# Kernel optimization log

Measured on AMD Instinct MI355X. Metric: run time of the kernel, lower is better.

Reference implementation:

```python
import jax, jax.numpy as jnp
import numpy as np

B, N, SIG_DIM, K = 128, 200000, 192, 32


def _l2norm(x):
    return x / jnp.linalg.norm(x, axis=-1, keepdims=True)


def setup_inputs() -> dict:
    key = jax.random.key(0)
    kq, kg, km = jax.random.split(key, 3)
    # queries and gallery signatures are L2-normalised per the docstring
    query_signature = _l2norm(jax.random.normal(kq, (B, SIG_DIM), dtype=jnp.float32))
    gallery_sigs = _l2norm(jax.random.normal(kg, (N, SIG_DIM), dtype=jnp.float32))
    exclude_mask = jax.random.bernoulli(km, p=0.01, shape=(B, N))
    return {
        "query_signature": query_signature,
        "gallery_sigs": gallery_sigs,
        "exclude_mask": exclude_mask,
        "k": K,
    }


def reference(query_signature, gallery_sigs, exclude_mask, k):
    # Equivalent to the chunked running top-k merge in Gallery.retrieve:
    # cosine-sim scores (inputs pre-normalised), masked fill -inf, global top-k.
    scores = query_signature @ gallery_sigs.T              # [B, N]
    scores = jnp.where(exclude_mask, -jnp.inf, scores)
    top_scores, top_idx = jax.lax.top_k(scores, k)          # [B, k] each
    return top_idx.astype(jnp.int64), top_scores
```

## Files before the change

kernel.cpp:

```cpp
#include <hip/hip_runtime.h>
#include <hip/hip_bf16.h>
#include <cstdint>
#include <cstddef>

#define BQ 128
#define DK 192
#define KTOP 32
#define CHI 32
#define QCAP 512
#define CAP 8192
#define OCAP 65536
#define MARGIN 0.02f
#define SCN 768
#define THRV 3200

#define NEG_INF (-__builtin_huge_valf())

typedef short short8v __attribute__((ext_vector_type(8)));
typedef float f32x16  __attribute__((ext_vector_type(16)));

__device__ __forceinline__ unsigned fkey(float s) {
    unsigned u = __float_as_uint(s);
    return (u & 0x80000000u) ? ~u : (u | 0x80000000u);
}
__device__ __forceinline__ bool pri_gt(float s1, int i1, float s2, int i2) {
    return (s1 > s2) || (s1 == s2 && i1 < i2);
}
__device__ __forceinline__ unsigned pk_trunc(float a, float b) {
    return __builtin_amdgcn_perm(__float_as_uint(b), __float_as_uint(a),
                                 0x07060302u);
}
__device__ __forceinline__ unsigned f2bf_rne(float x) {
    unsigned u = __float_as_uint(x);
    unsigned r = u + 0x7FFFu + ((u >> 16) & 1u);
    return r >> 16;
}
__device__ __forceinline__ float dot192(const float* __restrict__ a,
                                        const float* __restrict__ b) {
    float s = 0.f;
    #pragma unroll 8
    for (int k = 0; k < DK; ++k) s = fmaf(a[k], b[k], s);
    return s;
}
__device__ __forceinline__ void gload_lds16(const void* g, void* l) {
    __builtin_amdgcn_global_load_lds(
        (const __attribute__((address_space(1))) unsigned int*)g,
        (__attribute__((address_space(3))) unsigned int*)l,
        16, 0, 0);
}

__global__ __launch_bounds__(256) void qprep(
    const float* __restrict__ Qf, unsigned short* __restrict__ Qb)
{
    const int i = blockIdx.x * 256 + threadIdx.x;
    if (i < BQ * DK) Qb[i] = (unsigned short)f2bf_rne(Qf[i]);
}

template<int MODE>
__global__ __launch_bounds__(256, 2) void score_pass(
    const float* __restrict__ Qf, const unsigned short* __restrict__ Qb,
    const float* __restrict__ G,
    const int* __restrict__ mask, const float* __restrict__ thrm,
    float* __restrict__ gmax,
    int* __restrict__ gcnt, float* __restrict__ cs, int* __restrict__ ci,
    int* __restrict__ ocnt, int* __restrict__ oq, int* __restrict__ og,
    float* __restrict__ osv,
    int Ntot, int NCH, int SC)
{
    __shared__ float    Gf[CHI * DK];
    __shared__ float    thrmS[BQ];
    __shared__ unsigned queue[QCAP];
    __shared__ int      qn;

    const int t = threadIdx.x;
    const int w = t >> 6, lane = t & 63;
    const int lo5 = lane & 31, hi = lane >> 5;
    const int qbW = w * 32;

    const int chunk = (MODE == 0)
        ? (int)(((long long)blockIdx.x * NCH) / SC)
        : (int)blockIdx.x;
    const int cb = chunk * CHI;

    #pragma unroll
    for (int i = 0; i < 6; ++i) {
        const int slot = t + (i << 8);
        const int r = slot / 48, c = slot - r * 48;
        size_t grow = (size_t)cb + r;
        if (grow >= (size_t)Ntot) grow = (size_t)Ntot - 1;
        const char* gp = (const char*)G + grow * (DK * 4) + ((c ^ (r & 7)) << 4);
        char* lp = (char*)Gf + ((i << 2) + w) * 1024;
        gload_lds16(gp, lp);
    }

    uint4 aF[12];
    {
        const unsigned short* qp = Qb + (size_t)(qbW + lo5) * DK + hi * 8;
        #pragma unroll
        for (int s = 0; s < 12; ++s)
            aF[s] = *reinterpret_cast<const uint4*>(qp + s * 16);
    }

    if (t < BQ) thrmS[t] = (MODE == 1) ? thrm[t] : 0.f;
    if (t == 0) qn = 0;
    __syncthreads();

    const unsigned xsh = (unsigned)((lo5 & 7) << 4);
    const char* rowp = (const char*)Gf + lo5 * (DK * 4);

    f32x16 acc = {0,0,0,0,0,0,0,0,0,0,0,0,0,0,0,0};
    #pragma unroll
    for (int s = 0; s < 12; ++s) {
        const unsigned b0 = ((unsigned)((s * 4 + hi * 2) << 4)) ^ xsh;
        const unsigned b1 = ((unsigned)((s * 4 + hi * 2 + 1) << 4)) ^ xsh;
        float4 f0 = *reinterpret_cast<const float4*>(rowp + b0);
        float4 f1 = *reinterpret_cast<const float4*>(rowp + b1);
        union { unsigned u[4]; short8v v; } bu;
        bu.u[0] = pk_trunc(f0.x, f0.y); bu.u[1] = pk_trunc(f0.z, f0.w);
        bu.u[2] = pk_trunc(f1.x, f1.y); bu.u[3] = pk_trunc(f1.z, f1.w);
        union { uint4 u; short8v v; } au; au.u = aF[s];
        acc = __builtin_amdgcn_mfma_f32_32x32x16_bf16(au.v, bu.v, acc, 0, 0, 0);
    }

    const int g = cb + lo5;
    if (MODE == 0) {
        #pragma unroll
        for (int j = 0; j < 16; ++j) {
            const int row = (j & 3) + 8 * (j >> 2) + 4 * hi;
            const int q = qbW + row;
            float m = NEG_INF;
            if (g < Ntot && !mask[(size_t)q * (size_t)Ntot + g])
                m = acc[j];
            #pragma unroll
            for (int off = 1; off < 32; off <<= 1)
                m = fmaxf(m, __shfl_xor(m, off));
            if (lo5 == 0) gmax[(size_t)blockIdx.x * BQ + q] = m;
        }
    } else {
        #pragma unroll
        for (int j = 0; j < 16; ++j) {
            const int row = (j & 3) + 8 * (j >> 2) + 4 * hi;
            const int q = qbW + row;
            const float th = thrmS[q];
            const float s = acc[j];
            if (g < Ntot && s >= th) {
                if (!mask[(size_t)q * (size_t)Ntot + g]) {
                    const int p = atomicAdd(&qn, 1);
                    if (p < QCAP) {
                        queue[p] = ((unsigned)q << 24) | (unsigned)g;
                    } else {
                        float sx = dot192(Qf + q * DK, G + (size_t)g * DK);
                        const int op = atomicAdd(ocnt, 1);
                        if (op < OCAP) { oq[op] = q; og[op] = g; osv[op] = sx; }
                    }
                }
            }
        }
        __syncthreads();
        const int nq = qn < QCAP ? qn : QCAP;
        for (int cc = w; cc < nq; cc += 4) {
            const unsigned pk = queue[cc];
            const int q = pk >> 24, gg = pk & 0xFFFFFF;
            const float* qr = Qf + q * DK;
            const float* gr = G + (size_t)gg * DK;
            const int k0 = lane * 3;
            float part = qr[k0] * gr[k0];
            part = fmaf(qr[k0 + 1], gr[k0 + 1], part);
            part = fmaf(qr[k0 + 2], gr[k0 + 2], part);
            #pragma unroll
            for (int off = 32; off > 0; off >>= 1)
                part += __shfl_xor(part, off);
            if (lane == 0) {
                const int pos = atomicAdd(&gcnt[q * 16], 1);
                if (pos < CAP) {
                    cs[(size_t)q * CAP + pos] = part;
                    ci[(size_t)q * CAP + pos] = gg;
                } else {
                    const int op = atomicAdd(ocnt, 1);
                    if (op < OCAP) { oq[op] = q; og[op] = gg; osv[op] = part; }
                }
            }
        }
    }
}

__global__ __launch_bounds__(256) void thr32(
    const float* __restrict__ gmax, float* __restrict__ thrm, int SC)
{
    __shared__ float vals[THRV];
    __shared__ int hist[256];
    __shared__ int hscan[256];
    __shared__ int bS, gtS;

    const int q = blockIdx.x;
    const int t = threadIdx.x;
    const int M = SC < THRV ? SC : THRV;

    for (int i = t; i < M; i += 256) {
        float m = gmax[(size_t)i * BQ + q];
        for (int j = i + THRV; j < SC; j += THRV)
            m = fmaxf(m, gmax[(size_t)j * BQ + q]);
        vals[i] = m;
    }
    __syncthreads();

    unsigned prefix = 0, pmask = 0;
    int kneed = KTOP;
    for (int pass = 0; pass < 4; ++pass) {
        const int shift = 24 - pass * 8;
        hist[t] = 0;
        __syncthreads();
        for (int i = t; i < M; i += 256) {
            unsigned k = fkey(vals[i]);
            if ((k & pmask) == prefix) atomicAdd(&hist[(k >> shift) & 255], 1);
        }
        __syncthreads();
        int* src = hist; int* dst = hscan;
        for (int off = 1; off < 256; off <<= 1) {
            int v = src[t] + ((t + off) < 256 ? src[t + off] : 0);
            __syncthreads();
            dst[t] = v;
            __syncthreads();
            int* tmp = src; src = dst; dst = tmp;
        }
        if (src[t] >= kneed && (t == 255 || src[t + 1] < kneed)) {
            bS = t; gtS = (t == 255) ? 0 : src[t + 1];
        }
        __syncthreads();
        kneed -= gtS;
        prefix |= ((unsigned)bS) << shift;
        pmask  |= 0xFFu << shift;
        __syncthreads();
    }
    if (t == 0) {
        unsigned u = (prefix & 0x80000000u) ? (prefix & 0x7FFFFFFFu) : ~prefix;
        thrm[q] = __uint_as_float(u) - MARGIN;
    }
}

__global__ __launch_bounds__(256) void select_topk(
    const float* __restrict__ cs, const int* __restrict__ ci,
    const int* __restrict__ gcnt,
    const int* __restrict__ ocnt, const int* __restrict__ oq,
    const int* __restrict__ og, const float* __restrict__ osv,
    float* __restrict__ out)
{
    __shared__ int   hist[256];
    __shared__ int   hscan[256];
    __shared__ float Ls[256];
    __shared__ int   Li[256];
    __shared__ int   lcnt, nTotS, bS, gtS;
    __shared__ float wrs[4]; __shared__ int wri[4], wrslot[4];

    const int q = blockIdx.x;
    const int t = threadIdx.x;
    const int n0 = gcnt[q * 16];
    const int n = n0 < CAP ? n0 : CAP;
    const size_t base = (size_t)q * CAP;
    const int novf0 = *ocnt;
    const int novf = novf0 < OCAP ? novf0 : OCAP;

    if (t == 0) nTotS = 0;
    __syncthreads();
    {
        int part = (t == 0) ? n : 0;
        for (int i = t; i < novf; i += 256)
            if (oq[i] == q) part++;
        atomicAdd(&nTotS, part);
    }
    __syncthreads();
    const int nTot = nTotS;

    unsigned prefix = 0, pmask = 0;
    int kneed = KTOP;

    if (nTot > KTOP) {
        for (int pass = 0; pass < 4; ++pass) {
            const int shift = 24 - pass * 8;
            hist[t] = 0;
            __syncthreads();
            for (int i = t; i < n; i += 256) {
                unsigned k = fkey(cs[base + i]);
                if ((k & pmask) == prefix)
                    atomicAdd(&hist[(k >> shift) & 255], 1);
            }
            for (int i = t; i < novf; i += 256) {
                if (oq[i] == q) {
                    unsigned k = fkey(osv[i]);
                    if ((k & pmask) == prefix)
                        atomicAdd(&hist[(k >> shift) & 255], 1);
                }
            }
            __syncthreads();
            int* src = hist; int* dst = hscan;
            for (int off = 1; off < 256; off <<= 1) {
                int v = src[t] + ((t + off) < 256 ? src[t + off] : 0);
                __syncthreads();
                dst[t] = v;
                __syncthreads();
                int* tmp = src; src = dst; dst = tmp;
            }
            if (src[t] >= kneed && (t == 255 || src[t + 1] < kneed)) {
                bS = t;
                gtS = (t == 255) ? 0 : src[t + 1];
            }
            __syncthreads();
            const int b = bS;
            kneed -= gtS;
            prefix |= ((unsigned)b) << shift;
            pmask  |= 0xFFu << shift;
            __syncthreads();
        }
    }

    if (t == 0) lcnt = 0;
    __syncthreads();
    const unsigned T = (nTot > KTOP) ? prefix : 0u;
    for (int i = t; i < n; i += 256) {
        float s = cs[base + i];
        if (fkey(s) >= T) {
            int p = atomicAdd(&lcnt, 1);
            if (p < 256) { Ls[p] = s; Li[p] = ci[base + i]; }
        }
    }
    for (int i = t; i < novf; i += 256) {
        if (oq[i] == q) {
            float s = osv[i];
            if (fkey(s) >= T) {
                int p = atomicAdd(&lcnt, 1);
                if (p < 256) { Ls[p] = s; Li[p] = og[i]; }
            }
        }
    }
    __syncthreads();
    const int M = lcnt < 256 ? lcnt : 256;

    const int w = t >> 6, lane = t & 63;
    for (int r = 0; r < KTOP; ++r) {
        float bv = (t < M) ? Ls[t] : NEG_INF;
        int   bi = (t < M) ? Li[t] : 0x7fffffff;
        int   bslot = t;
        #pragma unroll
        for (int off = 32; off > 0; off >>= 1) {
            float ov = __shfl_xor(bv, off);
            int   oi = __shfl_xor(bi, off);
            int   osl = __shfl_xor(bslot, off);
            if (pri_gt(ov, oi, bv, bi)) { bv = ov; bi = oi; bslot = osl; }
        }
        if (lane == 0) { wrs[w] = bv; wri[w] = bi; wrslot[w] = bslot; }
        __syncthreads();
        if (t == 0) {
            float fv = wrs[0]; int fi = wri[0]; int fs = wrslot[0];
            #pragma unroll
            for (int ww = 1; ww < 4; ++ww)
                if (pri_gt(wrs[ww], wri[ww], fv, fi)) {
                    fv = wrs[ww]; fi = wri[ww]; fs = wrslot[ww];
                }
            out[q * KTOP + r]                     = (float)fi;
            out[(size_t)BQ * KTOP + q * KTOP + r] = fv;
            Ls[fs] = NEG_INF; Li[fs] = 0x7fffffff;
        }
        __syncthreads();
    }
}

extern "C" void kernel_launch(void* const* d_in, const int* in_sizes, int n_in,
                              void* d_out, int out_size, void* d_ws, size_t ws_size,
                              hipStream_t stream)
{
    const float* Qf   = (const float*)d_in[0];
    const float* G    = (const float*)d_in[1];
    const int*   mask = (const int*)d_in[2];
    const int Ntot = in_sizes[1] / DK;

    const int NCH = (Ntot + CHI - 1) / CHI;
    int SC = SCN;
    if (SC > NCH) SC = NCH;

    char* w = (char*)d_ws;
    int*   ocnt = (int*)(w + 0);
    int*   gcnt = (int*)(w + 1024);
    float* thrm = (float*)(w + 10240);
    unsigned short* Qb = (unsigned short*)(w + 16384);
    size_t off = 16384 + (size_t)BQ * DK * 2;
    off = (off + 255) & ~(size_t)255;
    float* gmax = (float*)(w + off);
    off += (size_t)SC * BQ * 4; off = (off + 255) & ~(size_t)255;
    float* cs   = (float*)(w + off);
    off += (size_t)BQ * CAP * 4;
    int*   ci   = (int*)(w + off);
    off += (size_t)BQ * CAP * 4;
    int*   oqv  = (int*)(w + off);   off += (size_t)OCAP * 4;
    int*   ogv  = (int*)(w + off);   off += (size_t)OCAP * 4;
    float* osv  = (float*)(w + off);

    (void)hipMemsetAsync(w, 0, 16384, stream);
    qprep<<<dim3((BQ * DK + 255) / 256), dim3(256), 0, stream>>>(Qf, Qb);
    score_pass<0><<<dim3(SC), dim3(256), 0, stream>>>(
        Qf, Qb, G, mask, thrm, gmax, gcnt, cs, ci, ocnt, oqv, ogv, osv,
        Ntot, NCH, SC);
    thr32<<<dim3(BQ), dim3(256), 0, stream>>>(gmax, thrm, SC);
    score_pass<1><<<dim3(NCH), dim3(256), 0, stream>>>(
        Qf, Qb, G, mask, thrm, gmax, gcnt, cs, ci, ocnt, oqv, ogv, osv,
        Ntot, NCH, SC);
    select_topk<<<dim3(BQ), dim3(256), 0, stream>>>(
        cs, ci, gcnt, ocnt, oqv, ogv, osv, (float*)d_out);
}
```

Measured before the change: 144.2 us.

## Persistent double-buffered score pass with sharded candidates and deferred fp32 rescoring

Both score passes become persistent grid-stride loops that double-buffer gallery chunks in LDS with async global-to-LDS loads, overlapping the next chunk's fetch with the current MFMA. The query bf16 fragments are pre-laid-out in MFMA order so each lane loads them coalesced. Candidates are written with their bf16 scores into per-query, per-shard buffers, which spreads the atomic contention. The exact fp32 dot-product recomputation moves out of the score kernel into select_topk, which radix-selects a coarse cutoff minus a margin, rescored survivors, and selects again. This removes the per-block queue and in-loop fp32 dots at the cost of a heavier select kernel and bounded shard capacities.

```diff
diff --git a/kernel.cpp b/kernel.cpp
--- a/kernel.cpp
+++ b/kernel.cpp
@@ -7,12 +7,14 @@
 #define DK 192
 #define KTOP 32
 #define CHI 32
-#define QCAP 512
-#define CAP 8192
+#define NSH 64
+#define SCAP 256
+#define LCCAP 2048
 #define OCAP 65536
 #define MARGIN 0.02f
 #define SCN 768
 #define THRV 3200
+#define GRID1 768
 
 #define NEG_INF (-__builtin_huge_valf())
 
@@ -22,6 +24,10 @@
 __device__ __forceinline__ unsigned fkey(float s) {
     unsigned u = __float_as_uint(s);
     return (u & 0x80000000u) ? ~u : (u | 0x80000000u);
+}
+__device__ __forceinline__ float keyval(unsigned k) {
+    return (k & 0x80000000u) ? __uint_as_float(k & 0x7FFFFFFFu)
+                             : __uint_as_float(~k);
 }
 __device__ __forceinline__ bool pri_gt(float s1, int i1, float s2, int i2) {
     return (s1 > s2) || (s1 == s2 && i1 < i2);
@@ -50,16 +56,22 @@
 }
 
 __global__ __launch_bounds__(256) void qprep(
-    const float* __restrict__ Qf, unsigned short* __restrict__ Qb)
+    const float* __restrict__ Qf, unsigned short* __restrict__ Qi)
 {
-    const int i = blockIdx.x * 256 + threadIdx.x;
-    if (i < BQ * DK) Qb[i] = (unsigned short)f2bf_rne(Qf[i]);
+    const int b = blockIdx.x * 256 + threadIdx.x;
+    if (b >= 12 * 256) return;
+    const int s = b >> 8, w = (b >> 6) & 3, lane = b & 63;
+    const int q  = w * 32 + (lane & 31);
+    const int k0 = (lane >> 5) * 8 + s * 16;
+    const float* qp = Qf + q * DK + k0;
+    unsigned short* dst = Qi + (size_t)b * 8;
+    #pragma unroll
+    for (int e = 0; e < 8; ++e) dst[e] = (unsigned short)f2bf_rne(qp[e]);
 }
 
 template<int MODE>
 __global__ __launch_bounds__(256, 2) void score_pass(
-    const float* __restrict__ Qf, const unsigned short* __restrict__ Qb,
-    const float* __restrict__ G,
+    const unsigned short* __restrict__ Qi, const float* __restrict__ G,
     const int* __restrict__ mask, const float* __restrict__ thrm,
     float* __restrict__ gmax,
     int* __restrict__ gcnt, float* __restrict__ cs, int* __restrict__ ci,
@@ -67,120 +79,126 @@
     float* __restrict__ osv,
     int Ntot, int NCH, int SC)
 {
-    __shared__ float    Gf[CHI * DK];
-    __shared__ float    thrmS[BQ];
-    __shared__ unsigned queue[QCAP];
-    __shared__ int      qn;
+    __shared__ float Gf[2][CHI * DK];
+    __shared__ float thrmS[BQ];
 
     const int t = threadIdx.x;
     const int w = t >> 6, lane = t & 63;
     const int lo5 = lane & 31, hi = lane >> 5;
     const int qbW = w * 32;
-
-    const int chunk = (MODE == 0)
-        ? (int)(((long long)blockIdx.x * NCH) / SC)
-        : (int)blockIdx.x;
-    const int cb = chunk * CHI;
-
-    #pragma unroll
-    for (int i = 0; i < 6; ++i) {
-        const int slot = t + (i << 8);
-        const int r = slot / 48, c = slot - r * 48;
-        size_t grow = (size_t)cb + r;
-        if (grow >= (size_t)Ntot) grow = (size_t)Ntot - 1;
-        const char* gp = (const char*)G + grow * (DK * 4) + ((c ^ (r & 7)) << 4);
-        char* lp = (char*)Gf + ((i << 2) + w) * 1024;
-        gload_lds16(gp, lp);
-    }
+    const int shard = blockIdx.x & (NSH - 1);
 
     uint4 aF[12];
     {
-        const unsigned short* qp = Qb + (size_t)(qbW + lo5) * DK + hi * 8;
+        const uint4* qp = reinterpret_cast<const uint4*>(Qi) + (w << 6) + lane;
+        #pragma unroll
+        for (int s = 0; s < 12; ++s) aF[s] = qp[s << 8];
+    }
+    #pragma unroll
+    for (int s = 0; s < 12; ++s)
+        asm volatile("" : "+v"(aF[s].x), "+v"(aF[s].y),
+                          "+v"(aF[s].z), "+v"(aF[s].w));
+
+    if (t < BQ) thrmS[t] = (MODE == 1) ? thrm[t] : 0.f;
+
+    const int limit  = (MODE == 0) ? SC : NCH;
+    const int stride = (int)gridDim.x;
+
+    auto CHUNK_OF = [&](int si) {
+        return (MODE == 0) ? (int)(((long long)si * NCH) / SC) : si;
+    };
+    auto ISSUE = [&](int chunk, int buf) {
+        const size_t cbase = (size_t)chunk * CHI;
+        #pragma unroll
+        for (int i = 0; i < 6; ++i) {
+            const int slot = t + (i << 8);
+            const int r = slot / 48, c = slot - r * 48;
+            size_t grow = cbase + r;
+            if (grow >= (size_t)Ntot) grow = (size_t)Ntot - 1;
+            const char* gp = (const char*)G + grow * (DK * 4)
+                           + ((c ^ (r & 7)) << 4);
+            char* lp = (char*)&Gf[buf][0] + ((i << 2) + w) * 1024;
+            gload_lds16(gp, lp);
+        }
+    };
+
+    int si = blockIdx.x;
+    if (si < limit) ISSUE(CHUNK_OF(si), 0);
+    __syncthreads();
+    int cur = 0;
+
+    const unsigned xsh = (unsigned)((lo5 & 7) << 4);
+
+    while (si < limit) {
+        const int chunk = CHUNK_OF(si);
+        const int cb = chunk * CHI;
+        const int nx = si + stride;
+        const bool more = nx < limit;
+        if (more) ISSUE(CHUNK_OF(nx), cur ^ 1);
+
+        if (more) asm volatile("s_waitcnt vmcnt(6)" ::: "memory");
+        else      asm volatile("s_waitcnt vmcnt(0)" ::: "memory");
+        __builtin_amdgcn_sched_barrier(0);
+        __builtin_amdgcn_s_barrier();
+
         #pragma unroll
         for (int s = 0; s < 12; ++s)
-            aF[s] = *reinterpret_cast<const uint4*>(qp + s * 16);
-    }
-
-    if (t < BQ) thrmS[t] = (MODE == 1) ? thrm[t] : 0.f;
-    if (t == 0) qn = 0;
-    __syncthreads();
-
-    const unsigned xsh = (unsigned)((lo5 & 7) << 4);
-    const char* rowp = (const char*)Gf + lo5 * (DK * 4);
-
-    f32x16 acc = {0,0,0,0,0,0,0,0,0,0,0,0,0,0,0,0};
-    #pragma unroll
-    for (int s = 0; s < 12; ++s) {
-        const unsigned b0 = ((unsigned)((s * 4 + hi * 2) << 4)) ^ xsh;
-        const unsigned b1 = ((unsigned)((s * 4 + hi * 2 + 1) << 4)) ^ xsh;
-        float4 f0 = *reinterpret_cast<const float4*>(rowp + b0);
-        float4 f1 = *reinterpret_cast<const float4*>(rowp + b1);
-        union { unsigned u[4]; short8v v; } bu;
-        bu.u[0] = pk_trunc(f0.x, f0.y); bu.u[1] = pk_trunc(f0.z, f0.w);
-        bu.u[2] = pk_trunc(f1.x, f1.y); bu.u[3] = pk_trunc(f1.z, f1.w);
-        union { uint4 u; short8v v; } au; au.u = aF[s];
-        acc = __builtin_amdgcn_mfma_f32_32x32x16_bf16(au.v, bu.v, acc, 0, 0, 0);
-    }
-
-    const int g = cb + lo5;
-    if (MODE == 0) {
+            asm volatile("" : "+v"(aF[s].x), "+v"(aF[s].y),
+                              "+v"(aF[s].z), "+v"(aF[s].w));
+
+        const char* rowp = (const char*)&Gf[cur][0] + lo5 * (DK * 4);
+        f32x16 acc = {0,0,0,0,0,0,0,0,0,0,0,0,0,0,0,0};
         #pragma unroll
-        for (int j = 0; j < 16; ++j) {
-            const int row = (j & 3) + 8 * (j >> 2) + 4 * hi;
-            const int q = qbW + row;
-            float m = NEG_INF;
-            if (g < Ntot && !mask[(size_t)q * (size_t)Ntot + g])
-                m = acc[j];
+        for (int s = 0; s < 12; ++s) {
+            const unsigned b0 = ((unsigned)((s * 4 + hi * 2) << 4)) ^ xsh;
+            const unsigned b1 = ((unsigned)((s * 4 + hi * 2 + 1) << 4)) ^ xsh;
+            float4 f0 = *reinterpret_cast<const float4*>(rowp + b0);
+            float4 f1 = *reinterpret_cast<const float4*>(rowp + b1);
+            union { unsigned u[4]; short8v v; } bu;
+            bu.u[0] = pk_trunc(f0.x, f0.y); bu.u[1] = pk_trunc(f0.z, f0.w);
+            bu.u[2] = pk_trunc(f1.x, f1.y); bu.u[3] = pk_trunc(f1.z, f1.w);
+            union { uint4 u; short8v v; } au; au.u = aF[s];
+            acc = __builtin_amdgcn_mfma_f32_32x32x16_bf16(au.v, bu.v, acc, 0, 0, 0);
+        }
+
+        const int g = cb + lo5;
+        if (MODE == 0) {
             #pragma unroll
-            for (int off = 1; off < 32; off <<= 1)
-                m = fmaxf(m, __shfl_xor(m, off));
-            if (lo5 == 0) gmax[(size_t)blockIdx.x * BQ + q] = m;
-        }
-    } else {
-        #pragma unroll
-        for (int j = 0; j < 16; ++j) {
-            const int row = (j & 3) + 8 * (j >> 2) + 4 * hi;
-            const int q = qbW + row;
-            const float th = thrmS[q];
-            const float s = acc[j];
-            if (g < Ntot && s >= th) {
-                if (!mask[(size_t)q * (size_t)Ntot + g]) {
-                    const int p = atomicAdd(&qn, 1);
-                    if (p < QCAP) {
-                        queue[p] = ((unsigned)q << 24) | (unsigned)g;
-                    } else {
-                        float sx = dot192(Qf + q * DK, G + (size_t)g * DK);
-                        const int op = atomicAdd(ocnt, 1);
-                        if (op < OCAP) { oq[op] = q; og[op] = g; osv[op] = sx; }
+            for (int j = 0; j < 16; ++j) {
+                const int row = (j & 3) + 8 * (j >> 2) + 4 * hi;
+                const int q = qbW + row;
+                float m = NEG_INF;
+                if (g < Ntot && !mask[(size_t)q * (size_t)Ntot + g])
+                    m = acc[j];
+                #pragma unroll
+                for (int off = 1; off < 32; off <<= 1)
+                    m = fmaxf(m, __shfl_xor(m, off));
+                if (lo5 == 0) gmax[(size_t)si * BQ + q] = m;
+            }
+        } else {
+            #pragma unroll
+            for (int j = 0; j < 16; ++j) {
+                const int row = (j & 3) + 8 * (j >> 2) + 4 * hi;
+                const int q = qbW + row;
+                const float s = acc[j];
+                if (g < Ntot && s >= thrmS[q]) {
+                    if (!mask[(size_t)q * (size_t)Ntot + g]) {
+                        const int cidx = q * NSH + shard;
+                        const int pos = atomicAdd(&gcnt[cidx * 16], 1);
+                        if (pos < SCAP) {
+                            const size_t o = (size_t)cidx * SCAP + pos;
+                            cs[o] = s; ci[o] = g;
+                        } else {
+                            const int op = atomicAdd(ocnt, 1);
+                            if (op < OCAP) { oq[op] = q; og[op] = g; osv[op] = s; }
+                        }
                     }
                 }
             }
         }
-        __syncthreads();
-        const int nq = qn < QCAP ? qn : QCAP;
-        for (int cc = w; cc < nq; cc += 4) {
-            const unsigned pk = queue[cc];
-            const int q = pk >> 24, gg = pk & 0xFFFFFF;
-            const float* qr = Qf + q * DK;
-            const float* gr = G + (size_t)gg * DK;
-            const int k0 = lane * 3;
-            float part = qr[k0] * gr[k0];
-            part = fmaf(qr[k0 + 1], gr[k0 + 1], part);
-            part = fmaf(qr[k0 + 2], gr[k0 + 2], part);
-            #pragma unroll
-            for (int off = 32; off > 0; off >>= 1)
-                part += __shfl_xor(part, off);
-            if (lane == 0) {
-                const int pos = atomicAdd(&gcnt[q * 16], 1);
-                if (pos < CAP) {
-                    cs[(size_t)q * CAP + pos] = part;
-                    ci[(size_t)q * CAP + pos] = gg;
-                } else {
-                    const int op = atomicAdd(ocnt, 1);
-                    if (op < OCAP) { oq[op] = q; og[op] = gg; osv[op] = part; }
-                }
-            }
-        }
+        __builtin_amdgcn_s_barrier();
+        cur ^= 1;
+        si = nx;
     }
 }
 
@@ -232,38 +250,41 @@
         pmask  |= 0xFFu << shift;
         __syncthreads();
     }
-    if (t == 0) {
-        unsigned u = (prefix & 0x80000000u) ? (prefix & 0x7FFFFFFFu) : ~prefix;
-        thrm[q] = __uint_as_float(u) - MARGIN;
-    }
+    if (t == 0) thrm[q] = keyval(prefix) - MARGIN;
 }
 
 __global__ __launch_bounds__(256) void select_topk(
+    const float* __restrict__ Qf, const float* __restrict__ G,
     const float* __restrict__ cs, const int* __restrict__ ci,
     const int* __restrict__ gcnt,
     const int* __restrict__ ocnt, const int* __restrict__ oq,
     const int* __restrict__ og, const float* __restrict__ osv,
     float* __restrict__ out)
 {
+    __shared__ int   cnts[NSH];
     __shared__ int   hist[256];
     __shared__ int   hscan[256];
+    __shared__ int   Lc[LCCAP];
+    __shared__ float Lr[LCCAP];
     __shared__ float Ls[256];
     __shared__ int   Li[256];
-    __shared__ int   lcnt, nTotS, bS, gtS;
+    __shared__ int   lcS, lfS, nTotS, bS, gtS;
     __shared__ float wrs[4]; __shared__ int wri[4], wrslot[4];
 
     const int q = blockIdx.x;
     const int t = threadIdx.x;
-    const int n0 = gcnt[q * 16];
-    const int n = n0 < CAP ? n0 : CAP;
-    const size_t base = (size_t)q * CAP;
+    const size_t qbase = (size_t)q * NSH * SCAP;
     const int novf0 = *ocnt;
     const int novf = novf0 < OCAP ? novf0 : OCAP;
 
+    if (t < NSH) {
+        int v = gcnt[(q * NSH + t) * 16];
+        cnts[t] = v < SCAP ? v : SCAP;
+    }
     if (t == 0) nTotS = 0;
     __syncthreads();
     {
-        int part = (t == 0) ? n : 0;
+        int part = (t < NSH) ? cnts[t] : 0;
         for (int i = t; i < novf; i += 256)
             if (oq[i] == q) part++;
         atomicAdd(&nTotS, part);
@@ -273,16 +294,18 @@
 
     unsigned prefix = 0, pmask = 0;
     int kneed = KTOP;
-
     if (nTot > KTOP) {
         for (int pass = 0; pass < 4; ++pass) {
             const int shift = 24 - pass * 8;
             hist[t] = 0;
             __syncthreads();
-            for (int i = t; i < n; i += 256) {
-                unsigned k = fkey(cs[base + i]);
-                if ((k & pmask) == prefix)
-                    atomicAdd(&hist[(k >> shift) & 255], 1);
+            for (int i = t; i < NSH * SCAP; i += 256) {
+                const int sh = i >> 8, sl = i & (SCAP - 1);
+                if (sl < cnts[sh]) {
+                    unsigned k = fkey(cs[qbase + i]);
+                    if ((k & pmask) == prefix)
+                        atomicAdd(&hist[(k >> shift) & 255], 1);
+                }
             }
             for (int i = t; i < novf; i += 256) {
                 if (oq[i] == q) {
@@ -301,39 +324,83 @@
                 int* tmp = src; src = dst; dst = tmp;
             }
             if (src[t] >= kneed && (t == 255 || src[t + 1] < kneed)) {
-                bS = t;
-                gtS = (t == 255) ? 0 : src[t + 1];
-            }
-            __syncthreads();
-            const int b = bS;
+                bS = t; gtS = (t == 255) ? 0 : src[t + 1];
+            }
+            __syncthreads();
             kneed -= gtS;
-            prefix |= ((unsigned)b) << shift;
+            prefix |= ((unsigned)bS) << shift;
             pmask  |= 0xFFu << shift;
             __syncthreads();
         }
     }
-
-    if (t == 0) lcnt = 0;
-    __syncthreads();
-    const unsigned T = (nTot > KTOP) ? prefix : 0u;
-    for (int i = t; i < n; i += 256) {
-        float s = cs[base + i];
-        if (fkey(s) >= T) {
-            int p = atomicAdd(&lcnt, 1);
-            if (p < 256) { Ls[p] = s; Li[p] = ci[base + i]; }
+    const float cutoff = (nTot > KTOP) ? (keyval(prefix) - MARGIN) : NEG_INF;
+
+    if (t == 0) lcS = 0;
+    __syncthreads();
+    for (int i = t; i < NSH * SCAP; i += 256) {
+        const int sh = i >> 8, sl = i & (SCAP - 1);
+        if (sl < cnts[sh]) {
+            if (cs[qbase + i] >= cutoff) {
+                int p = atomicAdd(&lcS, 1);
+                if (p < LCCAP) Lc[p] = ci[qbase + i];
+            }
         }
     }
     for (int i = t; i < novf; i += 256) {
-        if (oq[i] == q) {
-            float s = osv[i];
-            if (fkey(s) >= T) {
-                int p = atomicAdd(&lcnt, 1);
-                if (p < 256) { Ls[p] = s; Li[p] = og[i]; }
-            }
-        }
-    }
-    __syncthreads();
-    const int M = lcnt < 256 ? lcnt : 256;
+        if (oq[i] == q && osv[i] >= cutoff) {
+            int p = atomicAdd(&lcS, 1);
+            if (p < LCCAP) Lc[p] = og[i];
+        }
+    }
+    __syncthreads();
+    const int lc = lcS < LCCAP ? lcS : LCCAP;
+
+    for (int e = t; e < lc; e += 256)
+        Lr[e] = dot192(Qf + q * DK, G + (size_t)Lc[e] * DK);
+    __syncthreads();
+
+    unsigned p2 = 0, m2 = 0;
+    kneed = KTOP;
+    if (lc > KTOP) {
+        for (int pass = 0; pass < 4; ++pass) {
+            const int shift = 24 - pass * 8;
+            hist[t] = 0;
+            __syncthreads();
+            for (int e = t; e < lc; e += 256) {
+                unsigned k = fkey(Lr[e]);
+                if ((k & m2) == p2) atomicAdd(&hist[(k >> shift) & 255], 1);
+            }
+            __syncthreads();
+            int* src = hist; int* dst = hscan;
+            for (int off = 1; off < 256; off <<= 1) {
+                int v = src[t] + ((t + off) < 256 ? src[t + off] : 0);
+                __syncthreads();
+                dst[t] = v;
+                __syncthreads();
+                int* tmp = src; src = dst; dst = tmp;
+            }
+            if (src[t] >= kneed && (t == 255 || src[t + 1] < kneed)) {
+                bS = t; gtS = (t == 255) ? 0 : src[t + 1];
+            }
+            __syncthreads();
+            kneed -= gtS;
+            p2 |= ((unsigned)bS) << shift;
+            m2 |= 0xFFu << shift;
+            __syncthreads();
+        }
+    }
+    const unsigned T2 = (lc > KTOP) ? p2 : 0u;
+
+    if (t == 0) lfS = 0;
+    __syncthreads();
+    for (int e = t; e < lc; e += 256) {
+        if (fkey(Lr[e]) >= T2) {
+            int p = atomicAdd(&lfS, 1);
+            if (p < 256) { Ls[p] = Lr[e]; Li[p] = Lc[e]; }
+        }
+    }
+    __syncthreads();
+    const int M = lfS < 256 ? lfS : 256;
 
     const int w = t >> 6, lane = t & 63;
     for (int r = 0; r < KTOP; ++r) {
@@ -379,30 +446,32 @@
 
     char* w = (char*)d_ws;
     int*   ocnt = (int*)(w + 0);
-    int*   gcnt = (int*)(w + 1024);
-    float* thrm = (float*)(w + 10240);
-    unsigned short* Qb = (unsigned short*)(w + 16384);
-    size_t off = 16384 + (size_t)BQ * DK * 2;
+    int*   gcnt = (int*)(w + 4096);
+    const size_t gcnt_bytes = (size_t)BQ * NSH * 16 * 4;
+    size_t off = 4096 + gcnt_bytes;
+    float* thrm = (float*)(w + off);  off += 512;
     off = (off + 255) & ~(size_t)255;
+    unsigned short* Qi = (unsigned short*)(w + off);
+    off += (size_t)BQ * DK * 2; off = (off + 255) & ~(size_t)255;
     float* gmax = (float*)(w + off);
     off += (size_t)SC * BQ * 4; off = (off + 255) & ~(size_t)255;
     float* cs   = (float*)(w + off);
-    off += (size_t)BQ * CAP * 4;
+    off += (size_t)BQ * NSH * SCAP * 4;
     int*   ci   = (int*)(w + off);
-    off += (size_t)BQ * CAP * 4;
+    off += (size_t)BQ * NSH * SCAP * 4;
     int*   oqv  = (int*)(w + off);   off += (size_t)OCAP * 4;
     int*   ogv  = (int*)(w + off);   off += (size_t)OCAP * 4;
     float* osv  = (float*)(w + off);
 
-    (void)hipMemsetAsync(w, 0, 16384, stream);
-    qprep<<<dim3((BQ * DK + 255) / 256), dim3(256), 0, stream>>>(Qf, Qb);
-    score_pass<0><<<dim3(SC), dim3(256), 0, stream>>>(
-        Qf, Qb, G, mask, thrm, gmax, gcnt, cs, ci, ocnt, oqv, ogv, osv,
+    (void)hipMemsetAsync(w, 0, 4096 + gcnt_bytes, stream);
+    qprep<<<dim3(12), dim3(256), 0, stream>>>(Qf, Qi);
+    score_pass<0><<<dim3(256), dim3(256), 0, stream>>>(
+        Qi, G, mask, thrm, gmax, gcnt, cs, ci, ocnt, oqv, ogv, osv,
         Ntot, NCH, SC);
     thr32<<<dim3(BQ), dim3(256), 0, stream>>>(gmax, thrm, SC);
-    score_pass<1><<<dim3(NCH), dim3(256), 0, stream>>>(
-        Qf, Qb, G, mask, thrm, gmax, gcnt, cs, ci, ocnt, oqv, ogv, osv,
+    score_pass<1><<<dim3(GRID1), dim3(256), 0, stream>>>(
+        Qi, G, mask, thrm, gmax, gcnt, cs, ci, ocnt, oqv, ogv, osv,
         Ntot, NCH, SC);
     select_topk<<<dim3(BQ), dim3(256), 0, stream>>>(
-        cs, ci, gcnt, ocnt, oqv, ogv, osv, (float*)d_out);
-}
+        Qf, G, cs, ci, gcnt, ocnt, oqv, ogv, osv, (float*)d_out);
+}
```

New measurement: 248.3 us. +72.3%, slower.
